# Kernel tuning notes

Measured on AMD Instinct MI355X. Metric: run time of the kernel, lower is better.

Reference implementation:

```python
import jax, jax.numpy as jnp
import numpy as np

P = 512        # n_predicates
C = 65536      # n_constants
L = 1          # max_rule_length (only runnable config of original code)


def setup_inputs() -> dict:
    key = jax.random.key(0)
    k1, k2 = jax.random.split(key)
    initial_facts = jax.random.uniform(k1, (P, C), dtype=jnp.float32)
    rule_weights = jax.random.normal(k2, (P, L, P), dtype=jnp.float32)
    return {"initial_facts": initial_facts, "rule_weights": rule_weights, "n_iterations": 3}


def reference(initial_facts, rule_weights, n_iterations):
    # F.softmax(rule[step], dim=0) on the 1-D vector rule_weights[r, 0, :]
    # == softmax over the last axis of rule_weights[:, 0, :].
    # Stacking apply_rule over all rules r is exactly A @ facts.
    A = jax.nn.softmax(rule_weights[:, 0, :], axis=-1)  # [P, P]
    facts = initial_facts                                # [P, C]
    for _ in range(n_iterations):
        derived = A @ facts                              # [P, C] (rule r -> row r)
        facts = jnp.maximum(facts, derived.max(axis=0))  # broadcast [C] over [P, C]
    return facts
```

## Files before the change

kernel.cpp:

```cpp
#include <hip/hip_runtime.h>
#include <hip/hip_bf16.h>
#include <cstdint>


typedef __attribute__((ext_vector_type(8))) short bf16x8;
typedef __attribute__((ext_vector_type(8))) unsigned short u16x8;
typedef __attribute__((ext_vector_type(16))) float f32x16;
typedef unsigned short ushort_t;
typedef unsigned int uint32;

#define PDIM 512
#define CDIM 65536
#define NT   128
#define WAVES 16

__device__ __forceinline__ ushort_t f2bf(float x) {
    uint32 u = __float_as_uint(x);
    return (ushort_t)((u + 0x7fffu + ((u >> 16) & 1u)) >> 16);
}
__device__ __forceinline__ float bf2f(uint32 bits) { return __uint_as_float(bits << 16); }

__device__ __forceinline__ bf16x8 pkmax8(bf16x8 v, ushort_t mu) {
    u16x8 a = __builtin_bit_cast(u16x8, v);
    const u16x8 mb = {mu, mu, mu, mu, mu, mu, mu, mu};
    a = __builtin_elementwise_max(a, mb);
    return __builtin_bit_cast(bf16x8, a);
}

__global__ __launch_bounds__(64) void softmax_pack(const float* __restrict__ rw,
                                                   ushort_t* __restrict__ Apk) {
    const int r  = blockIdx.x;
    const int ln = threadIdx.x;
    const float* row = rw + r * PDIM;
    float4 x0 = *(const float4*)(row + ln * 8);
    float4 x1 = *(const float4*)(row + ln * 8 + 4);
    float v[8] = {x0.x, x0.y, x0.z, x0.w, x1.x, x1.y, x1.z, x1.w};

    float mx = -1e30f;
    #pragma unroll
    for (int i = 0; i < 8; ++i) mx = fmaxf(mx, v[i]);
    #pragma unroll
    for (int d = 1; d < 64; d <<= 1) mx = fmaxf(mx, __shfl_xor(mx, d, 64));
    float s = 0.f;
    #pragma unroll
    for (int i = 0; i < 8; ++i) { v[i] = __expf(v[i] - mx); s += v[i]; }
    #pragma unroll
    for (int d = 1; d < 64; d <<= 1) s += __shfl_xor(s, d, 64);
    const float inv = 1.f / s;

    ushort_t o[8];
    #pragma unroll
    for (int i = 0; i < 8; ++i) o[i] = f2bf(v[i] * inv);
    const int idx16 = ((ln >> 1) * 16 + (r >> 5)) * 64 + ((ln & 1) << 5) + (r & 31);
    *(int4*)(Apk + idx16 * 8) = *(const int4*)o;
}

__global__ __launch_bounds__(1024, 4) void ilp_kernel(
        const float* __restrict__ facts,
        const ushort_t* __restrict__ Apk,
        const int* __restrict__ n_iter_p,
        float* __restrict__ out) {
    __shared__ ushort_t ft[64 * NT * 8];
    __shared__ float wred[2][WAVES][NT];
    __shared__ float mfin[NT];

    const int tid  = threadIdx.x;
    const int wave = tid >> 6;
    const int lane = tid & 63;
    const int l31  = lane & 31;
    const int half = lane >> 5;
    const int c0   = blockIdx.x * NT;

    int n_iter = *n_iter_p;
    n_iter = n_iter < 0 ? 0 : (n_iter > 8 ? 8 : n_iter);

    {
        const int c   = tid & 127;
        const int grp = tid >> 7;
        #pragma unroll 2
        for (int s = 0; s < 8; ++s) {
            const int g = grp * 8 + s;
            ushort_t gb[8];
            #pragma unroll
            for (int i = 0; i < 8; ++i)
                gb[i] = f2bf(facts[(g * 8 + i) * CDIM + c0 + c]);
            *(int4*)(&ft[(g * NT + c) * 8]) = *(const int4*)gb;
        }
    }

    const ushort_t* abase = Apk + (wave * 64 + half * 32 + l31) * 8;
    bf16x8 aF[2], bR[4];
    aF[0] = *(const bf16x8*)(abase);
    aF[1] = *(const bf16x8*)(abase + 8192);

    __syncthreads();

    const int bbase = (half * NT + l31) * 8;
    #pragma unroll
    for (int ct2 = 0; ct2 < 4; ++ct2)
        bR[ct2] = *(const bf16x8*)(&ft[bbase + ct2 * 256]);

    ushort_t ml[4] = {0, 0, 0, 0};
    float    mf[4] = {0.f, 0.f, 0.f, 0.f};

    #pragma unroll 1
    for (int it = 0; it < n_iter; ++it) {
        f32x16 acc[4];
        #pragma unroll
        for (int ct2 = 0; ct2 < 4; ++ct2)
            #pragma unroll
            for (int e = 0; e < 16; ++e) acc[ct2][e] = 0.f;

        #pragma unroll 2
        for (int kt2 = 0; kt2 < 32; ++kt2) {
            const int cur = kt2 & 1;

            bf16x8 bC[4];
            #pragma unroll
            for (int ct2 = 0; ct2 < 4; ++ct2) bC[ct2] = pkmax8(bR[ct2], ml[ct2]);

            {
                const int bo = bbase + ((kt2 + 1) & 31) * 2048;
                #pragma unroll
                for (int ct2 = 0; ct2 < 4; ++ct2)
                    bR[ct2] = *(const bf16x8*)(&ft[bo + ct2 * 256]);
            }

            __builtin_amdgcn_s_setprio(1);
            #pragma unroll
            for (int ct2 = 0; ct2 < 4; ++ct2)
                acc[ct2] = __builtin_amdgcn_mfma_f32_32x32x16_bf16(
                    aF[cur], bC[ct2], acc[ct2], 0, 0, 0);
            __builtin_amdgcn_s_setprio(0);

            aF[cur] = *(const bf16x8*)(abase + ((kt2 + 2) & 31) * 8192);
        }

        float mx[4];
        #pragma unroll
        for (int ct2 = 0; ct2 < 4; ++ct2) {
            float m0 = -1e30f;
            #pragma unroll
            for (int e = 0; e < 16; ++e) m0 = fmaxf(m0, acc[ct2][e]);
            m0 = fmaxf(m0, __shfl_xor(m0, 32, 64));
            mx[ct2] = m0;
        }
        const int buf = it & 1;
        if (half == 0) {
            #pragma unroll
            for (int ct2 = 0; ct2 < 4; ++ct2) wred[buf][wave][ct2 * 32 + l31] = mx[ct2];
        }
        __syncthreads();
        #pragma unroll
        for (int ct2 = 0; ct2 < 4; ++ct2) {
            const int c = ct2 * 32 + l31;
            float m = wred[buf][0][c];
            #pragma unroll
            for (int w = 1; w < WAVES; ++w) m = fmaxf(m, wred[buf][w][c]);
            mf[ct2] = fmaxf(mf[ct2], m);
            ml[ct2] = f2bf(mf[ct2]);
        }
    }

    if (wave == 0 && half == 0) {
        #pragma unroll
        for (int ct2 = 0; ct2 < 4; ++ct2) mfin[ct2 * 32 + l31] = mf[ct2];
    }
    __syncthreads();

    {
        const int c   = tid & 127;
        const int grp = tid >> 7;
        const float m = mfin[c];
        #pragma unroll 2
        for (int s = 0; s < 8; ++s) {
            const int g = grp * 8 + s;
            ushort_t gb[8];
            *(int4*)gb = *(const int4*)(&ft[(g * NT + c) * 8]);
            #pragma unroll
            for (int i = 0; i < 8; ++i)
                out[(g * 8 + i) * CDIM + c0 + c] = fmaxf(bf2f(gb[i]), m);
        }
    }
}

extern "C" void kernel_launch(void* const* d_in, const int* in_sizes, int n_in,
                              void* d_out, int out_size, void* d_ws, size_t ws_size,
                              hipStream_t stream) {
    const float* facts    = (const float*)d_in[0];
    const float* rw       = (const float*)d_in[1];
    const int*   n_iter_p = (const int*)d_in[2];
    float* out = (float*)d_out;

    ushort_t* Apk = (ushort_t*)d_ws;

    softmax_pack<<<PDIM, 64, 0, stream>>>(rw, Apk);
    ilp_kernel<<<CDIM / NT, 1024, 0, stream>>>(facts, Apk, n_iter_p, out);
}
```

Before: 332.1 us.

## Halve waves per block, give each wave two row tiles, apply max in LDS

The block drops from 16 to 8 waves, and each wave now computes two 32-row output tiles so every B fragment read from LDS feeds two MFMAs. The per-iteration max is no longer applied to B fragments in registers inside the inner loop. Instead it is folded into the LDS facts tile once per iteration with an extra barrier, and the running max state and the double-buffered reduction array are removed. This is meant to cut LDS traffic and the VALU packed-max work inside the MFMA loop, at the cost of fewer waves to hide latency and an extra full pass over LDS plus a sync each iteration.

After: 308.2 us. -7.2%, faster.

```diff
diff --git a/kernel.cpp b/kernel.cpp
--- a/kernel.cpp
+++ b/kernel.cpp
@@ -12,7 +12,7 @@
 #define PDIM 512
 #define CDIM 65536
 #define NT   128
-#define WAVES 16
+#define WAVES 8
 
 __device__ __forceinline__ ushort_t f2bf(float x) {
     uint32 u = __float_as_uint(x);
@@ -55,14 +55,13 @@
     *(int4*)(Apk + idx16 * 8) = *(const int4*)o;
 }
 
-__global__ __launch_bounds__(1024, 4) void ilp_kernel(
+__global__ __launch_bounds__(512, 2) void ilp_kernel(
         const float* __restrict__ facts,
         const ushort_t* __restrict__ Apk,
         const int* __restrict__ n_iter_p,
         float* __restrict__ out) {
     __shared__ ushort_t ft[64 * NT * 8];
-    __shared__ float wred[2][WAVES][NT];
-    __shared__ float mfin[NT];
+    __shared__ float wred[WAVES][NT];
 
     const int tid  = threadIdx.x;
     const int wave = tid >> 6;
@@ -74,12 +73,15 @@
     int n_iter = *n_iter_p;
     n_iter = n_iter < 0 ? 0 : (n_iter > 8 ? 8 : n_iter);
 
+    wred[wave][lane]      = 0.f;
+    wred[wave][lane + 64] = 0.f;
+
     {
         const int c   = tid & 127;
         const int grp = tid >> 7;
-        #pragma unroll 2
-        for (int s = 0; s < 8; ++s) {
-            const int g = grp * 8 + s;
+        #pragma unroll 4
+        for (int s = 0; s < 16; ++s) {
+            const int g = grp * 16 + s;
             ushort_t gb[8];
             #pragma unroll
             for (int i = 0; i < 8; ++i)
@@ -88,93 +90,99 @@
         }
     }
 
-    const ushort_t* abase = Apk + (wave * 64 + half * 32 + l31) * 8;
-    bf16x8 aF[2], bR[4];
-    aF[0] = *(const bf16x8*)(abase);
-    aF[1] = *(const bf16x8*)(abase + 8192);
+    const ushort_t* abase = Apk + wave * 1024 + (half * 32 + l31) * 8;
+    bf16x8 aF[2][2], bR[2][4];
+    aF[0][0] = *(const bf16x8*)(abase);
+    aF[0][1] = *(const bf16x8*)(abase + 512);
+    aF[1][0] = *(const bf16x8*)(abase + 8192);
+    aF[1][1] = *(const bf16x8*)(abase + 8192 + 512);
 
     __syncthreads();
 
     const int bbase = (half * NT + l31) * 8;
     #pragma unroll
-    for (int ct2 = 0; ct2 < 4; ++ct2)
-        bR[ct2] = *(const bf16x8*)(&ft[bbase + ct2 * 256]);
-
-    ushort_t ml[4] = {0, 0, 0, 0};
-    float    mf[4] = {0.f, 0.f, 0.f, 0.f};
+    for (int ct2 = 0; ct2 < 4; ++ct2) {
+        bR[0][ct2] = *(const bf16x8*)(&ft[bbase + ct2 * 256]);
+        bR[1][ct2] = *(const bf16x8*)(&ft[bbase + 2048 + ct2 * 256]);
+    }
 
     #pragma unroll 1
     for (int it = 0; it < n_iter; ++it) {
-        f32x16 acc[4];
+        f32x16 acc[2][4];
         #pragma unroll
-        for (int ct2 = 0; ct2 < 4; ++ct2)
-            #pragma unroll
-            for (int e = 0; e < 16; ++e) acc[ct2][e] = 0.f;
+        for (int rt2 = 0; rt2 < 2; ++rt2)
+            #pragma unroll
+            for (int ct2 = 0; ct2 < 4; ++ct2)
+                #pragma unroll
+                for (int e = 0; e < 16; ++e) acc[rt2][ct2][e] = 0.f;
 
         #pragma unroll 2
         for (int kt2 = 0; kt2 < 32; ++kt2) {
             const int cur = kt2 & 1;
 
-            bf16x8 bC[4];
-            #pragma unroll
-            for (int ct2 = 0; ct2 < 4; ++ct2) bC[ct2] = pkmax8(bR[ct2], ml[ct2]);
-
-            {
-                const int bo = bbase + ((kt2 + 1) & 31) * 2048;
-                #pragma unroll
-                for (int ct2 = 0; ct2 < 4; ++ct2)
-                    bR[ct2] = *(const bf16x8*)(&ft[bo + ct2 * 256]);
+            __builtin_amdgcn_s_setprio(1);
+            #pragma unroll
+            for (int ct2 = 0; ct2 < 4; ++ct2) {
+                acc[0][ct2] = __builtin_amdgcn_mfma_f32_32x32x16_bf16(
+                    aF[cur][0], bR[cur][ct2], acc[0][ct2], 0, 0, 0);
+                acc[1][ct2] = __builtin_amdgcn_mfma_f32_32x32x16_bf16(
+                    aF[cur][1], bR[cur][ct2], acc[1][ct2], 0, 0, 0);
             }
-
-            __builtin_amdgcn_s_setprio(1);
+            __builtin_amdgcn_s_setprio(0);
+
+            const int ktp = (kt2 + 2) & 31;
+            const ushort_t* ap = abase + ktp * 8192;
+            aF[cur][0] = *(const bf16x8*)(ap);
+            aF[cur][1] = *(const bf16x8*)(ap + 512);
+            const int bo = bbase + ktp * 2048;
             #pragma unroll
             for (int ct2 = 0; ct2 < 4; ++ct2)
-                acc[ct2] = __builtin_amdgcn_mfma_f32_32x32x16_bf16(
-                    aF[cur], bC[ct2], acc[ct2], 0, 0, 0);
-            __builtin_amdgcn_s_setprio(0);
-
-            aF[cur] = *(const bf16x8*)(abase + ((kt2 + 2) & 31) * 8192);
-        }
-
-        float mx[4];
+                bR[cur][ct2] = *(const bf16x8*)(&ft[bo + ct2 * 256]);
+        }
+
         #pragma unroll
         for (int ct2 = 0; ct2 < 4; ++ct2) {
             float m0 = -1e30f;
             #pragma unroll
-            for (int e = 0; e < 16; ++e) m0 = fmaxf(m0, acc[ct2][e]);
+            for (int rt2 = 0; rt2 < 2; ++rt2)
+                #pragma unroll
+                for (int e = 0; e < 16; ++e) m0 = fmaxf(m0, acc[rt2][ct2][e]);
             m0 = fmaxf(m0, __shfl_xor(m0, 32, 64));
-            mx[ct2] = m0;
-        }
-        const int buf = it & 1;
-        if (half == 0) {
-            #pragma unroll
-            for (int ct2 = 0; ct2 < 4; ++ct2) wred[buf][wave][ct2 * 32 + l31] = mx[ct2];
+            if (half == 0) wred[wave][ct2 * 32 + l31] = m0;
         }
         __syncthreads();
-        #pragma unroll
-        for (int ct2 = 0; ct2 < 4; ++ct2) {
-            const int c = ct2 * 32 + l31;
-            float m = wred[buf][0][c];
-            #pragma unroll
-            for (int w = 1; w < WAVES; ++w) m = fmaxf(m, wred[buf][w][c]);
-            mf[ct2] = fmaxf(mf[ct2], m);
-            ml[ct2] = f2bf(mf[ct2]);
-        }
-    }
-
-    if (wave == 0 && half == 0) {
-        #pragma unroll
-        for (int ct2 = 0; ct2 < 4; ++ct2) mfin[ct2 * 32 + l31] = mf[ct2];
-    }
-    __syncthreads();
+
+        if (it < n_iter - 1) {
+            const int c   = tid & 127;
+            const int grp = tid >> 7;
+            float m = wred[0][c];
+            #pragma unroll
+            for (int w = 1; w < WAVES; ++w) m = fmaxf(m, wred[w][c]);
+            const ushort_t mu = f2bf(m);
+            #pragma unroll
+            for (int s = 0; s < 16; ++s) {
+                const int idx = ((grp * 16 + s) * NT + c) * 8;
+                bf16x8 v = *(const bf16x8*)(&ft[idx]);
+                *(bf16x8*)(&ft[idx]) = pkmax8(v, mu);
+            }
+            __syncthreads();
+            #pragma unroll
+            for (int ct2 = 0; ct2 < 4; ++ct2) {
+                bR[0][ct2] = *(const bf16x8*)(&ft[bbase + ct2 * 256]);
+                bR[1][ct2] = *(const bf16x8*)(&ft[bbase + 2048 + ct2 * 256]);
+            }
+        }
+    }
 
     {
         const int c   = tid & 127;
         const int grp = tid >> 7;
-        const float m = mfin[c];
-        #pragma unroll 2
-        for (int s = 0; s < 8; ++s) {
-            const int g = grp * 8 + s;
+        float m = wred[0][c];
+        #pragma unroll
+        for (int w = 1; w < WAVES; ++w) m = fmaxf(m, wred[w][c]);
+        #pragma unroll 4
+        for (int s = 0; s < 16; ++s) {
+            const int g = grp * 16 + s;
             ushort_t gb[8];
             *(int4*)gb = *(const int4*)(&ft[(g * NT + c) * 8]);
             #pragma unroll
@@ -195,5 +203,5 @@
     ushort_t* Apk = (ushort_t*)d_ws;
 
     softmax_pack<<<PDIM, 64, 0, stream>>>(rw, Apk);
-    ilp_kernel<<<CDIM / NT, 1024, 0, stream>>>(facts, Apk, n_iter_p, out);
-}
+    ilp_kernel<<<CDIM / NT, 512, 0, stream>>>(facts, Apk, n_iter_p, out);
+}
```
